# Performance work log

Hardware: AMD Instinct MI355X
Metric: run time of the kernel (lower is better)

## Reference

```python
import jax, jax.numpy as jnp
import numpy as np

IN_CH, OUT_CH, K, STRIDE, PAD, NUM_POINTS = 16, 32, 3, 1, 1, 3
NUM_INPUTS = IN_CH * K * K  # 144
BATCH, H, W = 8, 32, 32


def setup_inputs() -> dict:
    key = jax.random.key(0)
    k1, k2, k3 = jax.random.split(key, 3)
    x = jax.random.normal(k1, (BATCH, IN_CH, H, W), dtype=jnp.float32)
    # sorted breakpoint positions per (input, output) pair in [-1, 1]
    base = jnp.linspace(-1.0, 1.0, NUM_POINTS, dtype=jnp.float32)
    jitter = 0.2 * (jax.random.uniform(k2, (NUM_INPUTS, OUT_CH, NUM_POINTS), dtype=jnp.float32) - 0.5) / NUM_POINTS
    positions = jnp.sort(base[None, None, :] + jitter, axis=-1)  # (I, O, P), sorted
    values = 0.1 * jax.random.normal(k3, (NUM_INPUTS, OUT_CH, NUM_POINTS), dtype=jnp.float32)
    return {"x": x, "positions": positions, "values": values}


def _gather_pt(table, idx):
    # table: (I, O, P), idx: (N, I, O) -> (N, I, O)
    return jnp.take_along_axis(table[None], idx[..., None], axis=-1)[..., 0]


def _piecewise(patches, positions, values):
    # patches: (N, I); positions/values: (I, O, P)
    P = positions.shape[-1]
    # bucket index: number of breakpoints <= x, clipped to a valid segment
    cmp = patches[:, :, None, None] >= positions[None]       # (N, I, O, P)
    idx = jnp.clip(cmp.sum(axis=-1) - 1, 0, P - 2)           # (N, I, O)
    pl = _gather_pt(positions, idx)
    pr = _gather_pt(positions, idx + 1)
    vl = _gather_pt(values, idx)
    vr = _gather_pt(values, idx + 1)
    t = (patches[:, :, None] - pl) / (pr - pl)               # (N, I, O)
    y = vl + t * (vr - vl)                                   # per-pair piecewise-linear value
    return y.sum(axis=1)                                     # (N, O): sum over input dims


def reference(x, positions, values):
    B, C, Hi, Wi = x.shape
    Ho = (Hi + 2 * PAD - K) // STRIDE + 1
    Wo = (Wi + 2 * PAD - K) // STRIDE + 1
    # im2col / unfold: (B, C*K*K, Ho, Wo) with (c, kh, kw) feature ordering like torch unfold
    patches = jax.lax.conv_general_dilated_patches(
        x, (K, K), (STRIDE, STRIDE), ((PAD, PAD), (PAD, PAD)))
    patches = patches.reshape(B, NUM_INPUTS, Ho * Wo).transpose(0, 2, 1).reshape(-1, NUM_INPUTS)
    out = _piecewise(patches, positions, values)             # (B*Ho*Wo, O)
    out = out.reshape(B, Ho * Wo, OUT_CH).transpose(0, 2, 1)
    return out.reshape(B, OUT_CH, Ho, Wo)
```

## Files before the change

kernel.cpp:

```cpp
#include <hip/hip_runtime.h>

#define IN_CH 16
#define OUT_CH 32
#define NUM_INPUTS 144
#define H_ 32
#define W_ 32
#define TILE_H 4
#define LDS_H 6
#define LDS_W 34
#define CHW (LDS_H * LDS_W)

typedef __attribute__((ext_vector_type(2))) float f32x2;

__global__ __launch_bounds__(256, 2) void apc_fused(
        const float* __restrict__ x,
        const float* __restrict__ pos,
        const float* __restrict__ val,
        float* __restrict__ out) {
    __shared__ float  lx[IN_CH * CHW];
    __shared__ float4 ltPM[2 * NUM_INPUTS];
    __shared__ f32x2  ltD [2 * NUM_INPUTS];
    __shared__ f32x2  ltB [2 * NUM_INPUTS];
    __shared__ float4 lred[128];

    int bx  = blockIdx.x;
    int b   = bx >> 3;
    int ho0 = (bx & 7) * TILE_H;
    int g   = blockIdx.y;
    int tid = threadIdx.x;

    for (int idx = tid; idx < IN_CH * CHW; idx += 256) {
        int c   = idx / CHW;
        int rem = idx - c * CHW;
        int r   = rem / LDS_W;
        int col = rem - r * LDS_W;
        int gr  = ho0 + r - 1;
        int gc  = col - 1;
        float v = 0.f;
        if ((unsigned)gr < (unsigned)H_ && (unsigned)gc < (unsigned)W_)
            v = x[((b * IN_CH + c) * H_ + gr) * W_ + gc];
        lx[idx] = v;
    }

    if (tid < NUM_INPUTS) {
        const float4* pp = (const float4*)(pos + tid * 96 + g * 12);
        const float4* vv = (const float4*)(val + tid * 96 + g * 12);
        float4 pA = pp[0], pB = pp[1], pC = pp[2];
        float4 vA = vv[0], vB = vv[1], vC = vv[2];
        float P[12] = {pA.x,pA.y,pA.z,pA.w, pB.x,pB.y,pB.z,pB.w, pC.x,pC.y,pC.z,pC.w};
        float V[12] = {vA.x,vA.y,vA.z,vA.w, vB.x,vB.y,vB.z,vB.w, vC.x,vC.y,vC.z,vC.w};
        float p1[4], m0[4], dm[4], b0[4];
        #pragma unroll
        for (int k = 0; k < 4; ++k) {
            float q0 = P[3*k], q1 = P[3*k+1], q2 = P[3*k+2];
            float w0 = V[3*k], w1 = V[3*k+1], w2 = V[3*k+2];
            float s0 = (w1 - w0) / (q1 - q0);
            float s1 = (w2 - w1) / (q2 - q1);
            p1[k] = q1; m0[k] = s0; dm[k] = s1 - s0; b0[k] = w0 - s0 * q0;
        }
        ltPM[tid]              = make_float4(p1[0], p1[1], m0[0], m0[1]);
        ltD [tid]              = (f32x2){dm[0], dm[1]};
        ltB [tid]              = (f32x2){b0[0], b0[1]};
        ltPM[NUM_INPUTS + tid] = make_float4(p1[2], p1[3], m0[2], m0[3]);
        ltD [NUM_INPUTS + tid] = (f32x2){dm[2], dm[3]};
        ltB [NUM_INPUTS + tid] = (f32x2){b0[2], b0[3]};
    }
    __syncthreads();

    int col  = tid & 31;
    int trow = (tid >> 5) & 1;
    int pgrp = (tid >> 6) & 1;
    int cs   = tid >> 7;
    int i0   = cs * 72;
    int tb0  = pgrp * NUM_INPUTS + i0;
    int base = (2 * trow) * LDS_W + col;
    int lane = tid & 63;

    f32x2 bb = ltB[tb0 + lane];
    if (lane < 8) bb += ltB[tb0 + 64 + lane];
    #pragma unroll
    for (int m = 1; m < 64; m <<= 1) {
        bb.x += __shfl_xor(bb.x, m);
        bb.y += __shfl_xor(bb.y, m);
    }

    f32x2 aA = {0,0}, hA = {0,0};
    f32x2 aB = {0,0}, hB = {0,0};
    const f32x2 zz = {0.f, 0.f};

    #pragma unroll
    for (int cc = 0; cc < 8; ++cc) {
        int c = cs * 8 + cc;
        #pragma unroll
        for (int kw = 0; kw < 3; ++kw) {
            float p0 = lx[c * CHW + base + 0 * LDS_W + kw];
            float p1 = lx[c * CHW + base + 1 * LDS_W + kw];
            float p2 = lx[c * CHW + base + 2 * LDS_W + kw];
            float p3 = lx[c * CHW + base + 3 * LDS_W + kw];
            float pa[4] = {p0, p1, p2, p3};
            #pragma unroll
            for (int kh = 0; kh < 3; ++kh) {
                int ti = pgrp * NUM_INPUTS + (c * 3 + kh) * 3 + kw;
                float4 q = ltPM[ti];
                f32x2  D = ltD[ti];
                f32x2  P = {q.x, q.y}, M = {q.z, q.w};
                f32x2 qA = {pa[kh],     pa[kh]};
                f32x2 qB = {pa[kh + 1], pa[kh + 1]};
                aA = __builtin_elementwise_fma(M, qA, aA);
                hA = __builtin_elementwise_fma(D, __builtin_elementwise_max(qA - P, zz), hA);
                aB = __builtin_elementwise_fma(M, qB, aB);
                hB = __builtin_elementwise_fma(D, __builtin_elementwise_max(qB - P, zz), hB);
            }
        }
    }

    f32x2 rA = aA + hA + bb;
    f32x2 rB = aB + hB + bb;

    if (cs == 1)
        lred[tid - 128] = make_float4(rA.x, rA.y, rB.x, rB.y);
    __syncthreads();
    if (cs == 0) {
        float4 q = lred[tid];
        rA.x += q.x; rA.y += q.y; rB.x += q.z; rB.y += q.w;
        int hoA = ho0 + 2 * trow;
        int o0  = 4 * g + 2 * pgrp;
        int HW  = H_ * W_;
        int ob  = ((b * OUT_CH + o0) * H_ + hoA) * W_ + col;
        out[ob          ] = rA.x;
        out[ob +      HW] = rA.y;
        out[ob + W_     ] = rB.x;
        out[ob + W_ + HW] = rB.y;
    }
}

extern "C" void kernel_launch(void* const* d_in, const int* in_sizes, int n_in,
                              void* d_out, int out_size, void* d_ws, size_t ws_size,
                              hipStream_t stream) {
    const float* x   = (const float*)d_in[0];
    const float* pos = (const float*)d_in[1];
    const float* val = (const float*)d_in[2];

    dim3 grid(64, 8);
    apc_fused<<<grid, 256, 0, stream>>>(x, pos, val, (float*)d_out);
}
```

Baseline: 66.87 us.

## Halve block size, compute four output rows per thread, reduce via shuffle

```diff
diff --git a/kernel.cpp b/kernel.cpp
--- a/kernel.cpp
+++ b/kernel.cpp
@@ -12,16 +12,15 @@
 
 typedef __attribute__((ext_vector_type(2))) float f32x2;
 
-__global__ __launch_bounds__(256, 2) void apc_fused(
+__global__ __launch_bounds__(128) void apc_fused(
         const float* __restrict__ x,
         const float* __restrict__ pos,
         const float* __restrict__ val,
         float* __restrict__ out) {
     __shared__ float  lx[IN_CH * CHW];
-    __shared__ float4 ltPM[2 * NUM_INPUTS];
-    __shared__ f32x2  ltD [2 * NUM_INPUTS];
-    __shared__ f32x2  ltB [2 * NUM_INPUTS];
-    __shared__ float4 lred[128];
+    __shared__ float4 ltPM[2 * 146];
+    __shared__ f32x2  ltD [2 * 146];
+    __shared__ f32x2  ltB [2 * 146];
 
     int bx  = blockIdx.x;
     int b   = bx >> 3;
@@ -29,7 +28,7 @@
     int g   = blockIdx.y;
     int tid = threadIdx.x;
 
-    for (int idx = tid; idx < IN_CH * CHW; idx += 256) {
+    for (int idx = tid; idx < IN_CH * CHW; idx += 128) {
         int c   = idx / CHW;
         int rem = idx - c * CHW;
         int r   = rem / LDS_W;
@@ -42,9 +41,9 @@
         lx[idx] = v;
     }
 
-    if (tid < NUM_INPUTS) {
-        const float4* pp = (const float4*)(pos + tid * 96 + g * 12);
-        const float4* vv = (const float4*)(val + tid * 96 + g * 12);
+    for (int i = tid; i < NUM_INPUTS; i += 128) {
+        const float4* pp = (const float4*)(pos + i * 96 + g * 12);
+        const float4* vv = (const float4*)(val + i * 96 + g * 12);
         float4 pA = pp[0], pB = pp[1], pC = pp[2];
         float4 vA = vv[0], vB = vv[1], vC = vv[2];
         float P[12] = {pA.x,pA.y,pA.z,pA.w, pB.x,pB.y,pB.z,pB.w, pC.x,pC.y,pC.z,pC.w};
@@ -58,79 +57,74 @@
             float s1 = (w2 - w1) / (q2 - q1);
             p1[k] = q1; m0[k] = s0; dm[k] = s1 - s0; b0[k] = w0 - s0 * q0;
         }
-        ltPM[tid]              = make_float4(p1[0], p1[1], m0[0], m0[1]);
-        ltD [tid]              = (f32x2){dm[0], dm[1]};
-        ltB [tid]              = (f32x2){b0[0], b0[1]};
-        ltPM[NUM_INPUTS + tid] = make_float4(p1[2], p1[3], m0[2], m0[3]);
-        ltD [NUM_INPUTS + tid] = (f32x2){dm[2], dm[3]};
-        ltB [NUM_INPUTS + tid] = (f32x2){b0[2], b0[3]};
+        int slot = (i < 72) ? i : (i + 1);
+        ltPM[slot]       = make_float4(p1[0], p1[1], m0[0], m0[1]);
+        ltD [slot]       = (f32x2){dm[0], dm[1]};
+        ltB [slot]       = (f32x2){b0[0], b0[1]};
+        ltPM[146 + slot] = make_float4(p1[2], p1[3], m0[2], m0[3]);
+        ltD [146 + slot] = (f32x2){dm[2], dm[3]};
+        ltB [146 + slot] = (f32x2){b0[2], b0[3]};
     }
     __syncthreads();
 
     int col  = tid & 31;
-    int trow = (tid >> 5) & 1;
-    int pgrp = (tid >> 6) & 1;
-    int cs   = tid >> 7;
-    int i0   = cs * 72;
-    int tb0  = pgrp * NUM_INPUTS + i0;
-    int base = (2 * trow) * LDS_W + col;
-    int lane = tid & 63;
+    int cs   = (tid >> 5) & 1;
+    int pgrp = tid >> 6;
+    int hl   = tid & 31;
+    int tb0  = pgrp * 146 + cs * 73;
+    int c0   = cs * 8;
 
-    f32x2 bb = ltB[tb0 + lane];
-    if (lane < 8) bb += ltB[tb0 + 64 + lane];
+    f32x2 bb = ltB[tb0 + hl];
+    bb += ltB[tb0 + 32 + hl];
+    if (hl < 8) bb += ltB[tb0 + 64 + hl];
     #pragma unroll
-    for (int m = 1; m < 64; m <<= 1) {
+    for (int m = 1; m < 32; m <<= 1) {
         bb.x += __shfl_xor(bb.x, m);
         bb.y += __shfl_xor(bb.y, m);
     }
 
-    f32x2 aA = {0,0}, hA = {0,0};
-    f32x2 aB = {0,0}, hB = {0,0};
+    f32x2 a[4] = {{0,0},{0,0},{0,0},{0,0}};
+    f32x2 h[4] = {{0,0},{0,0},{0,0},{0,0}};
     const f32x2 zz = {0.f, 0.f};
 
     #pragma unroll
     for (int cc = 0; cc < 8; ++cc) {
-        int c = cs * 8 + cc;
+        int c = c0 + cc;
         #pragma unroll
         for (int kw = 0; kw < 3; ++kw) {
-            float p0 = lx[c * CHW + base + 0 * LDS_W + kw];
-            float p1 = lx[c * CHW + base + 1 * LDS_W + kw];
-            float p2 = lx[c * CHW + base + 2 * LDS_W + kw];
-            float p3 = lx[c * CHW + base + 3 * LDS_W + kw];
-            float pa[4] = {p0, p1, p2, p3};
+            float pa[6];
+            #pragma unroll
+            for (int r = 0; r < 6; ++r)
+                pa[r] = lx[c * CHW + r * LDS_W + col + kw];
             #pragma unroll
             for (int kh = 0; kh < 3; ++kh) {
-                int ti = pgrp * NUM_INPUTS + (c * 3 + kh) * 3 + kw;
-                float4 q = ltPM[ti];
-                f32x2  D = ltD[ti];
+                int t = (cc * 3 + kh) * 3 + kw;
+                float4 q = ltPM[tb0 + t];
+                f32x2  D = ltD [tb0 + t];
                 f32x2  P = {q.x, q.y}, M = {q.z, q.w};
-                f32x2 qA = {pa[kh],     pa[kh]};
-                f32x2 qB = {pa[kh + 1], pa[kh + 1]};
-                aA = __builtin_elementwise_fma(M, qA, aA);
-                hA = __builtin_elementwise_fma(D, __builtin_elementwise_max(qA - P, zz), hA);
-                aB = __builtin_elementwise_fma(M, qB, aB);
-                hB = __builtin_elementwise_fma(D, __builtin_elementwise_max(qB - P, zz), hB);
+                #pragma unroll
+                for (int r = 0; r < 4; ++r) {
+                    f32x2 pv = {pa[r + kh], pa[r + kh]};
+                    a[r] = __builtin_elementwise_fma(M, pv, a[r]);
+                    h[r] = __builtin_elementwise_fma(
+                        D, __builtin_elementwise_max(pv - P, zz), h[r]);
+                }
             }
         }
     }
 
-    f32x2 rA = aA + hA + bb;
-    f32x2 rB = aB + hB + bb;
-
-    if (cs == 1)
-        lred[tid - 128] = make_float4(rA.x, rA.y, rB.x, rB.y);
-    __syncthreads();
-    if (cs == 0) {
-        float4 q = lred[tid];
-        rA.x += q.x; rA.y += q.y; rB.x += q.z; rB.y += q.w;
-        int hoA = ho0 + 2 * trow;
-        int o0  = 4 * g + 2 * pgrp;
-        int HW  = H_ * W_;
-        int ob  = ((b * OUT_CH + o0) * H_ + hoA) * W_ + col;
-        out[ob          ] = rA.x;
-        out[ob +      HW] = rA.y;
-        out[ob + W_     ] = rB.x;
-        out[ob + W_ + HW] = rB.y;
+    int o0 = 4 * g + 2 * pgrp;
+    int HW = H_ * W_;
+    #pragma unroll
+    for (int r = 0; r < 4; ++r) {
+        f32x2 s = a[r] + h[r] + bb;
+        s.x += __shfl_xor(s.x, 32);
+        s.y += __shfl_xor(s.y, 32);
+        if (cs == 0) {
+            int ob = ((b * OUT_CH + o0) * H_ + (ho0 + r)) * W_ + col;
+            out[ob     ] = s.x;
+            out[ob + HW] = s.y;
+        }
     }
 }
 
@@ -142,5 +136,5 @@
     const float* val = (const float*)d_in[2];
 
     dim3 grid(64, 8);
-    apc_fused<<<grid, 256, 0, stream>>>(x, pos, val, (float*)d_out);
+    apc_fused<<<grid, 128, 0, stream>>>(x, pos, val, (float*)d_out);
 }
```

Measured after the change: 102.1 us. +52.7%, slower.
